# Kernel optimization log

Measured on AMD Instinct MI355X. Metric: run time of the kernel, lower is better.

The kernel has to match this reference:

```python
import jax, jax.numpy as jnp
import numpy as np

L_SIDE = 32
N_PIX = 12 * L_SIDE * L_SIDE      # 12288 sphere pixels
N_VALID = N_PIX // 2              # theta <= pi/2 hemisphere (first half by construction)
A_TH, B_TH, C_TH = 0.03, 1.0, 1.0  # ellipsoid semi-axes (thickness, 1, 1)


def _sphere_angles(n):
    # Deterministic Fibonacci-lattice sphere sampling standing in for SphereHealpix.
    i = np.arange(n, dtype=np.float64)
    z = 1.0 - 2.0 * (i + 0.5) / n          # cos(theta), descending -> theta<=pi/2 iff i < n/2
    theta = np.arccos(z)
    phi = (i * np.pi * (3.0 - np.sqrt(5.0))) % (2.0 * np.pi)
    return theta.astype(np.float32), phi.astype(np.float32)


def _ellipse_valid():
    # Faithful translation of ReconstructionModel.ellipse_valid for the valid hemisphere.
    theta_all, phi_all = _sphere_angles(N_PIX)
    tv = theta_all[:N_VALID].astype(np.float32)
    pv = phi_all[:N_VALID].astype(np.float32)
    a, b, c = np.float32(A_TH), np.float32(B_TH), np.float32(C_TH)
    # cartesian coords of valid pixels (computed BEFORE the angle shift)
    xv = np.cos(pv) * np.sin(tv)
    yv = np.sin(pv) * np.sin(tv)
    # meshgrid(phi, x) / meshgrid(theta, y) with ij indexing -> angles vary on rows, coords on cols
    phi = ((pv + np.pi / 2) % (2 * np.pi)).astype(np.float32)[:, None]   # [Nv,1]
    theta = ((tv + np.pi / 2) % np.pi).astype(np.float32)[:, None]       # [Nv,1]
    x = xv[None, :]
    y = yv[None, :]
    x_c = np.sin(2 * theta) / 2 * np.cos(phi)
    y_c = -np.sin(2 * theta) / 2 * np.sin(phi)
    z_c = (np.cos(2 * theta) + 1) / 2
    r = np.sqrt(2 * (np.cos(2 * theta) + 1)) / 2 + np.float32(1e-5)
    a2, b2, c2 = a * a, b * b, c * c
    ct, st = np.cos(theta), np.sin(theta)
    cp, sp = np.cos(phi), np.sin(phi)
    ct2, ct4 = ct ** 2, ct ** 4
    cp2 = cp ** 2
    x2, y2 = x ** 2, y ** 2
    s2p = np.sin(2.0 * phi)
    with np.errstate(invalid='ignore'):
        S = (-b2 * ct2 + b2 * ct4 - b2 * y2 - c2 * x2
             + a2 * b2 * ct4 + b2 * c2 * ct2 - b2 * c2 * ct4
             - b2 * x2 * cp2 + b2 * y2 * cp2 + c2 * x2 * cp2 - c2 * y2 * cp2
             - a2 * x2 * ct2 + c2 * x2 * ct2
             + b2 * x * y * s2p - c2 * x * y * s2p
             + a2 * x2 * cp2 * ct2 - a2 * y2 * cp2 * ct2
             - c2 * x2 * cp2 * ct2 + c2 * y2 * cp2 * ct2
             + 2.0 * b2 * x * cp * ct * st - 2.0 * b2 * y * ct * sp * st
             + 2.0 * c2 * x * y * cp * ct2 * sp - 2.0 * a2 * x * y * cp * ct2 * sp)
        num = (a * c * np.sqrt(S)
               - a2 * b * ct2 + 2.0 * a2 * b * ct4
               + 2.0 * b * c2 * ct2 - 2.0 * b * c2 * ct4
               + a2 * b * x * cp * ct * st - b * c2 * x * cp * ct * st
               - a2 * b * y * ct * sp * st + b * c2 * y * ct * sp * st)
        den = b * (a2 * ct2 - c2 * ct2 + c2)
        z = num / den
        f = ((x - x_c) ** 2 + (y - y_c) ** 2 + (z - z_c) ** 2) / r ** 2
    f = np.where(np.isnan(f), np.float32(0.0), f)   # f[f != f] = 0
    return f.astype(np.float32)


def setup_inputs() -> dict:
    key = jax.random.key(0)
    x = jax.random.uniform(key, (8, 16, N_PIX), dtype=jnp.float32)
    all_responses = jnp.asarray(_ellipse_valid())   # [N_VALID, N_VALID]
    return {"x": x, "all_responses": all_responses}


def reference(x, all_responses):
    nv = all_responses.shape[0]
    # masked gather: theta <= pi/2 is exactly the first nv pixels by construction
    x_valid = x[:, :, :nv]                                   # [B,C,Nv]
    mixture = jnp.einsum('bcn,nm->bcm', x_valid, all_responses)
    mixture = jnp.clip(mixture, 0.0, 1.0)                    # mix='clip'
    # masked scatter back into zero buffer
    out = jnp.zeros_like(x).at[:, :, :nv].set(mixture)
    return out
```

## Files before the change

kernel.cpp:

```cpp
#include <hip/hip_runtime.h>
#include <hip/hip_bf16.h>


#define NPIX 12288
#define NV   6144
#define MR   128
#define BNW  32
#define KST  128
#define NSTR (NV / BNW)
#define PARTF ((size_t)MR * NV)

typedef __attribute__((ext_vector_type(8))) short bf16x8;
typedef __attribute__((ext_vector_type(4))) float f32x4;
typedef __attribute__((ext_vector_type(4))) unsigned u32x4;

__device__ __forceinline__ unsigned pk2(float lo, float hi) {
    __hip_bfloat162 h = __float22bfloat162_rn(make_float2(lo, hi));
    union { __hip_bfloat162 h; unsigned u; } v; v.h = h; return v.u;
}

__device__ __forceinline__ void gld16(const void* g, void* l) {
    __builtin_amdgcn_global_load_lds(
        (const __attribute__((address_space(1))) void*)g,
        (__attribute__((address_space(3))) void*)l, 16, 0, 0);
}

__global__ __launch_bounds__(256) void prep_kernel(const float* __restrict__ x,
                                                   unsigned short* __restrict__ abf) {
    int q = blockIdx.x * 256 + threadIdx.x;
    int m = q / (NV / 8);
    int r = q % (NV / 8);
    int k = r * 8;
    const float* src = x + (size_t)m * NPIX + k;
    f32x4 a = *(const f32x4*)(src);
    f32x4 b = *(const f32x4*)(src + 4);
    u32x4 o;
    o[0] = pk2(a[0], a[1]); o[1] = pk2(a[2], a[3]);
    o[2] = pk2(b[0], b[1]); o[3] = pk2(b[2], b[3]);
    *(u32x4*)(abf + (size_t)m * NV + k) = o;
}

__global__ __launch_bounds__(256) void trans_kernel(const float* __restrict__ R,
                                                    unsigned short* __restrict__ RT) {
    __shared__ float T[64][65];
    const int tid = threadIdx.x;
    const int kt = blockIdx.x % (NV / 64);
    const int nt = blockIdx.x / (NV / 64);
    const int k0 = kt * 64, n0 = nt * 64;
    const int colg = (tid & 15) * 4;
    const int rowb = tid >> 4;
    #pragma unroll
    for (int it = 0; it < 4; ++it) {
        const int row = it * 16 + rowb;
        f32x4 v = *(const f32x4*)(R + (size_t)(k0 + row) * NV + n0 + colg);
        #pragma unroll
        for (int j = 0; j < 4; ++j) T[colg + j][row] = v[j];
    }
    __syncthreads();
    const int n = tid >> 2, seg = tid & 3;
    float f[16];
    #pragma unroll
    for (int u = 0; u < 16; ++u) f[u] = T[n][seg * 16 + u];
    u32x4 o0, o1;
    o0[0] = pk2(f[0], f[1]);  o0[1] = pk2(f[2], f[3]);
    o0[2] = pk2(f[4], f[5]);  o0[3] = pk2(f[6], f[7]);
    o1[0] = pk2(f[8], f[9]);  o1[1] = pk2(f[10], f[11]);
    o1[2] = pk2(f[12], f[13]); o1[3] = pk2(f[14], f[15]);
    unsigned short* dst = RT + (size_t)(n0 + n) * NV + k0 + seg * 16;
    *(u32x4*)(dst) = o0;
    *(u32x4*)(dst + 8) = o1;
}

__global__ __launch_bounds__(256) void gemm2_kernel(
        const unsigned short* __restrict__ A,
        const unsigned short* __restrict__ RT,
        float* __restrict__ out, float* __restrict__ wpart) {
    __shared__ unsigned char Bs[2][8192];

    const int tid = threadIdx.x;
    const int w = tid >> 6, l = tid & 63;
    const int ln = l & 15, lg = l >> 4;
    const int chunk = blockIdx.x & 7;
    const int nb = blockIdx.x >> 3;
    const int n0 = nb * BNW;
    const int kbase = chunk * 768;
    const int nsi = 768 / KST;

    const int f0 = tid * 16, f1 = 4096 + tid * 16;
    const int n_0 = f0 >> 8, n_1 = f1 >> 8;
    const int ko0 = (f0 & 255) ^ ((n_0 & 7) << 4);
    const int ko1 = (f1 & 255) ^ ((n_1 & 7) << 4);
    const char* g0 = (const char*)(RT + (size_t)(n0 + n_0) * NV + kbase) + ko0;
    const char* g1 = (const char*)(RT + (size_t)(n0 + n_1) * NV + kbase) + ko1;

    size_t arow0 = (size_t)(w * 32 + ln) * NV + kbase + lg * 8;
    size_t arow1 = arow0 + (size_t)16 * NV;

    f32x4 acc[2][2];
    #pragma unroll
    for (int a = 0; a < 2; ++a)
        #pragma unroll
        for (int b = 0; b < 2; ++b) {
            acc[a][b][0] = 0.f; acc[a][b][1] = 0.f;
            acc[a][b][2] = 0.f; acc[a][b][3] = 0.f;
        }

    gld16(g0, &Bs[0][f0]);
    gld16(g1, &Bs[0][f1]);
    __syncthreads();

    const int swn = (ln & 7) << 4;
    #pragma unroll 1
    for (int t = 0; t < nsi; ++t) {
        if (t + 1 < nsi) {
            const int nb2 = (t + 1) & 1;
            gld16(g0 + (t + 1) * 256, &Bs[nb2][f0]);
            gld16(g1 + (t + 1) * 256, &Bs[nb2][f1]);
        }
        const unsigned char* buf = Bs[t & 1];
        bf16x8 afr[2][4];
        #pragma unroll
        for (int ks = 0; ks < 4; ++ks) {
            afr[0][ks] = *(const bf16x8*)(A + arow0 + ks * 32);
            afr[1][ks] = *(const bf16x8*)(A + arow1 + ks * 32);
        }
        #pragma unroll
        for (int nt = 0; nt < 2; ++nt) {
            const int rowb = (nt * 16 + ln) * 256;
            #pragma unroll
            for (int ks = 0; ks < 4; ++ks) {
                bf16x8 bfr = *(const bf16x8*)(buf + rowb + (((lg * 16) + ks * 64) ^ swn));
                acc[0][nt] = __builtin_amdgcn_mfma_f32_16x16x32_bf16(afr[0][ks], bfr, acc[0][nt], 0, 0, 0);
                acc[1][nt] = __builtin_amdgcn_mfma_f32_16x16x32_bf16(afr[1][ks], bfr, acc[1][nt], 0, 0, 0);
            }
        }
        arow0 += KST; arow1 += KST;
        __syncthreads();
    }

    float* dst;
    size_t rstride;
    if (chunk < 2) { dst = out + (size_t)chunk * NV; rstride = NPIX; }
    else           { dst = wpart + (size_t)(chunk - 2) * PARTF; rstride = NV; }
    #pragma unroll
    for (int mt = 0; mt < 2; ++mt) {
        const int mbase = w * 32 + mt * 16 + lg * 4;
        #pragma unroll
        for (int nt = 0; nt < 2; ++nt) {
            const size_t cb = (size_t)(n0 + nt * 16 + ln);
            #pragma unroll
            for (int j = 0; j < 4; ++j)
                dst[(size_t)(mbase + j) * rstride + cb] = acc[mt][nt][j];
        }
    }
}

__device__ __forceinline__ bf16x8 cvt8(f32x4 a, f32x4 b) {
    union { unsigned u[4]; bf16x8 v; } r;
    r.u[0] = pk2(a[0], a[1]); r.u[1] = pk2(a[2], a[3]);
    r.u[2] = pk2(b[0], b[1]); r.u[3] = pk2(b[2], b[3]);
    return r.v;
}

__device__ __forceinline__ void sload(const float*& bptr, float2 (&r)[8]) {
    #pragma unroll
    for (int gi = 0; gi < 4; ++gi) {
        const float* p = bptr + (size_t)(gi * 32) * NV;
        r[2 * gi]     = *(const float2*)(p);
        r[2 * gi + 1] = *(const float2*)(p + NV);
    }
    bptr += (size_t)KST * NV;
}

__device__ __forceinline__ void wstage(unsigned char* buf, const float2 (&r)[8],
                                       int kq, int nq, int sw0, int sw1) {
    #pragma unroll
    for (int gi = 0; gi < 4; ++gi) {
        unsigned lo = pk2(r[2 * gi].x, r[2 * gi + 1].x);
        unsigned hi = pk2(r[2 * gi].y, r[2 * gi + 1].y);
        const int kbyte = (kq + gi * 32) * 2;
        *(unsigned*)(buf + nq * 256       + (kbyte ^ sw0)) = lo;
        *(unsigned*)(buf + (nq + 1) * 256 + (kbyte ^ sw1)) = hi;
    }
}

__device__ __forceinline__ void compute_fb(const unsigned char* buf,
        const float* __restrict__ X, size_t arow0, size_t arow1,
        int ln, int lg, f32x4 (&acc)[2][2]) {
    bf16x8 afr[2][4];
    #pragma unroll
    for (int ks = 0; ks < 4; ++ks) {
        f32x4 p0 = *(const f32x4*)(X + arow0 + ks * 32);
        f32x4 p1 = *(const f32x4*)(X + arow0 + ks * 32 + 4);
        afr[0][ks] = cvt8(p0, p1);
        f32x4 q0 = *(const f32x4*)(X + arow1 + ks * 32);
        f32x4 q1 = *(const f32x4*)(X + arow1 + ks * 32 + 4);
        afr[1][ks] = cvt8(q0, q1);
    }
    const int swn = (ln & 7) << 4;
    #pragma unroll
    for (int nt = 0; nt < 2; ++nt) {
        const int rowb = (nt * 16 + ln) * 256;
        #pragma unroll
        for (int ks = 0; ks < 4; ++ks) {
            bf16x8 bfr = *(const bf16x8*)(buf + rowb + (((lg * 16) + ks * 64) ^ swn));
            acc[0][nt] = __builtin_amdgcn_mfma_f32_16x16x32_bf16(afr[0][ks], bfr, acc[0][nt], 0, 0, 0);
            acc[1][nt] = __builtin_amdgcn_mfma_f32_16x16x32_bf16(afr[1][ks], bfr, acc[1][nt], 0, 0, 0);
        }
    }
}

__global__ __launch_bounds__(256) void gemm_fb_kernel(const float* __restrict__ X,
        const float* __restrict__ R, float* __restrict__ out) {
    __shared__ unsigned char Bs0[32 * 256];
    __shared__ unsigned char Bs1[32 * 256];
    const int tid = threadIdx.x;
    const int w = tid >> 6, l = tid & 63;
    const int ln = l & 15, lg = l >> 4;
    const int chunk = blockIdx.x / NSTR;
    const int nb = blockIdx.x % NSTR;
    const int n0 = nb * BNW;
    const int kbase = chunk * (NV / 2);
    const int nsi = (NV / 2) / KST;
    const int kq = (tid >> 4) * 2;
    const int nq = (tid & 15) * 2;
    const float* bptr = R + (size_t)(kbase + kq) * NV + (n0 + nq);
    const int sw0 = (nq & 7) << 4;
    const int sw1 = ((nq + 1) & 7) << 4;
    size_t arow0 = (size_t)(w * 32 + ln) * NPIX + kbase + lg * 8;
    size_t arow1 = arow0 + (size_t)16 * NPIX;
    f32x4 acc[2][2];
    #pragma unroll
    for (int a = 0; a < 2; ++a)
        #pragma unroll
        for (int b = 0; b < 2; ++b) {
            acc[a][b][0] = 0.f; acc[a][b][1] = 0.f;
            acc[a][b][2] = 0.f; acc[a][b][3] = 0.f;
        }
    float2 ring0[8], ring1[8];
    sload(bptr, ring0);
    sload(bptr, ring1);
    wstage(Bs0, ring0, kq, nq, sw0, sw1);
    __syncthreads();
    #pragma unroll 1
    for (int it = 0; it < nsi / 2; ++it) {
        const int s = it * 2;
        if (s + 2 < nsi) sload(bptr, ring0);
        compute_fb(Bs0, X, arow0, arow1, ln, lg, acc);
        arow0 += KST; arow1 += KST;
        wstage(Bs1, ring1, kq, nq, sw0, sw1);
        __syncthreads();
        if (s + 3 < nsi) sload(bptr, ring1);
        compute_fb(Bs1, X, arow0, arow1, ln, lg, acc);
        arow0 += KST; arow1 += KST;
        if (s + 2 < nsi) wstage(Bs0, ring0, kq, nq, sw0, sw1);
        __syncthreads();
    }
    float* dst = out + (size_t)chunk * NV;
    #pragma unroll
    for (int mt = 0; mt < 2; ++mt) {
        const int mbase = w * 32 + mt * 16 + lg * 4;
        #pragma unroll
        for (int nt = 0; nt < 2; ++nt) {
            const size_t cb = (size_t)(n0 + nt * 16 + ln);
            #pragma unroll
            for (int j = 0; j < 4; ++j)
                dst[(size_t)(mbase + j) * NPIX + cb] = acc[mt][nt][j];
        }
    }
}

__global__ __launch_bounds__(256) void reduce_kernel(float* __restrict__ out,
        const float* __restrict__ wpart, int nextra) {
    int q = blockIdx.x * 256 + threadIdx.x;
    int m = q / (NV / 4);
    int r = q % (NV / 4);
    size_t base = (size_t)m * NPIX + r * 4;
    f32x4 a = *(f32x4*)(out + base);
    f32x4 b = *(f32x4*)(out + base + NV);
    #pragma unroll
    for (int i = 0; i < 4; ++i) a[i] += b[i];
    #pragma unroll 1
    for (int p = 0; p < nextra; ++p) {
        f32x4 c = *(const f32x4*)(wpart + (size_t)p * PARTF + (size_t)m * NV + r * 4);
        #pragma unroll
        for (int i = 0; i < 4; ++i) a[i] += c[i];
    }
    f32x4 cz, z;
    #pragma unroll
    for (int i = 0; i < 4; ++i) {
        cz[i] = fminf(fmaxf(a[i], 0.f), 1.f);
        z[i] = 0.f;
    }
    *(f32x4*)(out + base) = cz;
    *(f32x4*)(out + base + NV) = z;
}

extern "C" void kernel_launch(void* const* d_in, const int* in_sizes, int n_in,
                              void* d_out, int out_size, void* d_ws, size_t ws_size,
                              hipStream_t stream) {
    const float* x = (const float*)d_in[0];
    const float* R = (const float*)d_in[1];
    float* out = (float*)d_out;

    const size_t abytes  = (size_t)MR * NV * 2;
    const size_t rtbytes = (size_t)NV * NV * 2;
    const size_t pbytes  = 6 * PARTF * 4;

    if (ws_size >= abytes + rtbytes + pbytes) {
        unsigned short* abf = (unsigned short*)d_ws;
        unsigned short* rt  = (unsigned short*)((char*)d_ws + abytes);
        float* wpart = (float*)((char*)d_ws + abytes + rtbytes);
        prep_kernel<<<(MR * NV / 8) / 256, 256, 0, stream>>>(x, abf);
        trans_kernel<<<(NV / 64) * (NV / 64), 256, 0, stream>>>(R, rt);
        gemm2_kernel<<<NSTR * 8, 256, 0, stream>>>(abf, rt, out, wpart);
        reduce_kernel<<<(MR * NV / 4) / 256, 256, 0, stream>>>(out, wpart, 6);
    } else {
        gemm_fb_kernel<<<NSTR * 2, 256, 0, stream>>>(x, R, out);
        reduce_kernel<<<(MR * NV / 4) / 256, 256, 0, stream>>>(out, nullptr, 0);
    }
}
```

Baseline: 278.6 us.

## Widen GEMM N tile, pad leading dims, rewrite transpose without LDS

The transpose kernel now reads eight rows of R per thread with vector loads and writes packed bf16 columns directly, with no shared-memory staging. The bf16 buffers and partials use a padded leading dimension of 6208 so that row strides avoid cache and channel aliasing. The GEMM tile grows from 32 to 64 N columns per block, so each A fragment is reused across more MFMAs, and the block count halves. All eight K-chunks now write partials to the workspace and a single reduce sums them, clamps and zero-fills, at the cost of more partial-buffer traffic and a larger workspace requirement.

```diff
diff --git a/kernel.cpp b/kernel.cpp
--- a/kernel.cpp
+++ b/kernel.cpp
@@ -5,10 +5,11 @@
 #define NPIX 12288
 #define NV   6144
 #define MR   128
-#define BNW  32
 #define KST  128
-#define NSTR (NV / BNW)
-#define PARTF ((size_t)MR * NV)
+#define LDK  6208
+#define LDA  6208
+#define LDP  6208
+#define PARTF ((size_t)MR * LDP)
 
 typedef __attribute__((ext_vector_type(8))) short bf16x8;
 typedef __attribute__((ext_vector_type(4))) float f32x4;
@@ -37,76 +38,71 @@
     u32x4 o;
     o[0] = pk2(a[0], a[1]); o[1] = pk2(a[2], a[3]);
     o[2] = pk2(b[0], b[1]); o[3] = pk2(b[2], b[3]);
-    *(u32x4*)(abf + (size_t)m * NV + k) = o;
+    *(u32x4*)(abf + (size_t)m * LDA + k) = o;
 }
 
 __global__ __launch_bounds__(256) void trans_kernel(const float* __restrict__ R,
                                                     unsigned short* __restrict__ RT) {
-    __shared__ float T[64][65];
     const int tid = threadIdx.x;
-    const int kt = blockIdx.x % (NV / 64);
-    const int nt = blockIdx.x / (NV / 64);
-    const int k0 = kt * 64, n0 = nt * 64;
-    const int colg = (tid & 15) * 4;
-    const int rowb = tid >> 4;
-    #pragma unroll
-    for (int it = 0; it < 4; ++it) {
-        const int row = it * 16 + rowb;
-        f32x4 v = *(const f32x4*)(R + (size_t)(k0 + row) * NV + n0 + colg);
-        #pragma unroll
-        for (int j = 0; j < 4; ++j) T[colg + j][row] = v[j];
-    }
-    __syncthreads();
-    const int n = tid >> 2, seg = tid & 3;
-    float f[16];
-    #pragma unroll
-    for (int u = 0; u < 16; ++u) f[u] = T[n][seg * 16 + u];
-    u32x4 o0, o1;
-    o0[0] = pk2(f[0], f[1]);  o0[1] = pk2(f[2], f[3]);
-    o0[2] = pk2(f[4], f[5]);  o0[3] = pk2(f[6], f[7]);
-    o1[0] = pk2(f[8], f[9]);  o1[1] = pk2(f[10], f[11]);
-    o1[2] = pk2(f[12], f[13]); o1[3] = pk2(f[14], f[15]);
-    unsigned short* dst = RT + (size_t)(n0 + n) * NV + k0 + seg * 16;
-    *(u32x4*)(dst) = o0;
-    *(u32x4*)(dst + 8) = o1;
+    const int w = tid >> 6, l = tid & 63;
+    const int band = blockIdx.x % 192;
+    const int nc   = blockIdx.x / 192;
+    const int k0 = band * 32 + w * 8;
+    const int n0 = nc * 256 + l * 4;
+    const float* src = R + (size_t)k0 * NV + n0;
+    f32x4 r[8];
+    #pragma unroll
+    for (int j = 0; j < 8; ++j) r[j] = *(const f32x4*)(src + (size_t)j * NV);
+    #pragma unroll
+    for (int c = 0; c < 4; ++c) {
+        u32x4 o;
+        o[0] = pk2(r[0][c], r[1][c]);
+        o[1] = pk2(r[2][c], r[3][c]);
+        o[2] = pk2(r[4][c], r[5][c]);
+        o[3] = pk2(r[6][c], r[7][c]);
+        *(u32x4*)(RT + (size_t)(n0 + c) * LDK + k0) = o;
+    }
 }
 
 __global__ __launch_bounds__(256) void gemm2_kernel(
         const unsigned short* __restrict__ A,
         const unsigned short* __restrict__ RT,
-        float* __restrict__ out, float* __restrict__ wpart) {
-    __shared__ unsigned char Bs[2][8192];
+        float* __restrict__ wpart) {
+    __shared__ unsigned char Bs[2][16384];
 
     const int tid = threadIdx.x;
     const int w = tid >> 6, l = tid & 63;
     const int ln = l & 15, lg = l >> 4;
     const int chunk = blockIdx.x & 7;
     const int nb = blockIdx.x >> 3;
-    const int n0 = nb * BNW;
+    const int n0 = nb * 64;
     const int kbase = chunk * 768;
     const int nsi = 768 / KST;
 
-    const int f0 = tid * 16, f1 = 4096 + tid * 16;
-    const int n_0 = f0 >> 8, n_1 = f1 >> 8;
-    const int ko0 = (f0 & 255) ^ ((n_0 & 7) << 4);
-    const int ko1 = (f1 & 255) ^ ((n_1 & 7) << 4);
-    const char* g0 = (const char*)(RT + (size_t)(n0 + n_0) * NV + kbase) + ko0;
-    const char* g1 = (const char*)(RT + (size_t)(n0 + n_1) * NV + kbase) + ko1;
-
-    size_t arow0 = (size_t)(w * 32 + ln) * NV + kbase + lg * 8;
-    size_t arow1 = arow0 + (size_t)16 * NV;
-
-    f32x4 acc[2][2];
+    int fo[4], nn[4];
+    const char* gg[4];
+    #pragma unroll
+    for (int i = 0; i < 4; ++i) {
+        fo[i] = tid * 16 + i * 4096;
+        nn[i] = fo[i] >> 8;
+        const int ko = (fo[i] & 255) ^ ((nn[i] & 7) << 4);
+        gg[i] = (const char*)(RT + (size_t)(n0 + nn[i]) * LDK + kbase) + ko;
+    }
+
+    size_t arow0 = (size_t)(w * 32 + ln) * LDA + kbase + lg * 8;
+    size_t arow1 = arow0 + (size_t)16 * LDA;
+
+    f32x4 acc[2][4];
     #pragma unroll
     for (int a = 0; a < 2; ++a)
         #pragma unroll
-        for (int b = 0; b < 2; ++b) {
+        for (int b = 0; b < 4; ++b) {
             acc[a][b][0] = 0.f; acc[a][b][1] = 0.f;
             acc[a][b][2] = 0.f; acc[a][b][3] = 0.f;
         }
 
-    gld16(g0, &Bs[0][f0]);
-    gld16(g1, &Bs[0][f1]);
+    #pragma unroll
+    for (int i = 0; i < 4; ++i) gld16(gg[i], &Bs[0][fo[i]]);
     __syncthreads();
 
     const int swn = (ln & 7) << 4;
@@ -114,8 +110,8 @@
     for (int t = 0; t < nsi; ++t) {
         if (t + 1 < nsi) {
             const int nb2 = (t + 1) & 1;
-            gld16(g0 + (t + 1) * 256, &Bs[nb2][f0]);
-            gld16(g1 + (t + 1) * 256, &Bs[nb2][f1]);
+            #pragma unroll
+            for (int i = 0; i < 4; ++i) gld16(gg[i] + (t + 1) * 256, &Bs[nb2][fo[i]]);
         }
         const unsigned char* buf = Bs[t & 1];
         bf16x8 afr[2][4];
@@ -125,7 +121,7 @@
             afr[1][ks] = *(const bf16x8*)(A + arow1 + ks * 32);
         }
         #pragma unroll
-        for (int nt = 0; nt < 2; ++nt) {
+        for (int nt = 0; nt < 4; ++nt) {
             const int rowb = (nt * 16 + ln) * 256;
             #pragma unroll
             for (int ks = 0; ks < 4; ++ks) {
@@ -138,41 +134,61 @@
         __syncthreads();
     }
 
-    float* dst;
-    size_t rstride;
-    if (chunk < 2) { dst = out + (size_t)chunk * NV; rstride = NPIX; }
-    else           { dst = wpart + (size_t)(chunk - 2) * PARTF; rstride = NV; }
+    float* dst = wpart + (size_t)chunk * PARTF;
     #pragma unroll
     for (int mt = 0; mt < 2; ++mt) {
         const int mbase = w * 32 + mt * 16 + lg * 4;
         #pragma unroll
-        for (int nt = 0; nt < 2; ++nt) {
+        for (int nt = 0; nt < 4; ++nt) {
             const size_t cb = (size_t)(n0 + nt * 16 + ln);
             #pragma unroll
             for (int j = 0; j < 4; ++j)
-                dst[(size_t)(mbase + j) * rstride + cb] = acc[mt][nt][j];
-        }
-    }
-}
-
+                dst[(size_t)(mbase + j) * LDP + cb] = acc[mt][nt][j];
+        }
+    }
+}
+
+__global__ __launch_bounds__(256) void reduce_kernel(float* __restrict__ out,
+        const float* __restrict__ wpart) {
+    int q = blockIdx.x * 256 + threadIdx.x;
+    int m = q / (NV / 4);
+    int r = q % (NV / 4);
+    f32x4 a;
+    a[0] = 0.f; a[1] = 0.f; a[2] = 0.f; a[3] = 0.f;
+    #pragma unroll 1
+    for (int p = 0; p < 8; ++p) {
+        f32x4 c = *(const f32x4*)(wpart + (size_t)p * PARTF + (size_t)m * LDP + r * 4);
+        #pragma unroll
+        for (int i = 0; i < 4; ++i) a[i] += c[i];
+    }
+    f32x4 cz, z;
+    #pragma unroll
+    for (int i = 0; i < 4; ++i) {
+        cz[i] = fminf(fmaxf(a[i], 0.f), 1.f);
+        z[i] = 0.f;
+    }
+    size_t base = (size_t)m * NPIX + r * 4;
+    *(f32x4*)(out + base) = cz;
+    *(f32x4*)(out + base + NV) = z;
+}
+
+typedef float2 fl2;
 __device__ __forceinline__ bf16x8 cvt8(f32x4 a, f32x4 b) {
     union { unsigned u[4]; bf16x8 v; } r;
     r.u[0] = pk2(a[0], a[1]); r.u[1] = pk2(a[2], a[3]);
     r.u[2] = pk2(b[0], b[1]); r.u[3] = pk2(b[2], b[3]);
     return r.v;
 }
-
-__device__ __forceinline__ void sload(const float*& bptr, float2 (&r)[8]) {
+__device__ __forceinline__ void sload(const float*& bptr, fl2 (&r)[8]) {
     #pragma unroll
     for (int gi = 0; gi < 4; ++gi) {
         const float* p = bptr + (size_t)(gi * 32) * NV;
-        r[2 * gi]     = *(const float2*)(p);
-        r[2 * gi + 1] = *(const float2*)(p + NV);
+        r[2 * gi]     = *(const fl2*)(p);
+        r[2 * gi + 1] = *(const fl2*)(p + NV);
     }
     bptr += (size_t)KST * NV;
 }
-
-__device__ __forceinline__ void wstage(unsigned char* buf, const float2 (&r)[8],
+__device__ __forceinline__ void wstage(unsigned char* buf, const fl2 (&r)[8],
                                        int kq, int nq, int sw0, int sw1) {
     #pragma unroll
     for (int gi = 0; gi < 4; ++gi) {
@@ -183,7 +199,6 @@
         *(unsigned*)(buf + (nq + 1) * 256 + (kbyte ^ sw1)) = hi;
     }
 }
-
 __device__ __forceinline__ void compute_fb(const unsigned char* buf,
         const float* __restrict__ X, size_t arow0, size_t arow1,
         int ln, int lg, f32x4 (&acc)[2][2]) {
@@ -209,7 +224,6 @@
         }
     }
 }
-
 __global__ __launch_bounds__(256) void gemm_fb_kernel(const float* __restrict__ X,
         const float* __restrict__ R, float* __restrict__ out) {
     __shared__ unsigned char Bs0[32 * 256];
@@ -217,9 +231,9 @@
     const int tid = threadIdx.x;
     const int w = tid >> 6, l = tid & 63;
     const int ln = l & 15, lg = l >> 4;
-    const int chunk = blockIdx.x / NSTR;
-    const int nb = blockIdx.x % NSTR;
-    const int n0 = nb * BNW;
+    const int chunk = blockIdx.x / 192;
+    const int nb = blockIdx.x % 192;
+    const int n0 = nb * 32;
     const int kbase = chunk * (NV / 2);
     const int nsi = (NV / 2) / KST;
     const int kq = (tid >> 4) * 2;
@@ -237,7 +251,7 @@
             acc[a][b][0] = 0.f; acc[a][b][1] = 0.f;
             acc[a][b][2] = 0.f; acc[a][b][3] = 0.f;
         }
-    float2 ring0[8], ring1[8];
+    fl2 ring0[8], ring1[8];
     sload(bptr, ring0);
     sload(bptr, ring1);
     wstage(Bs0, ring0, kq, nq, sw0, sw1);
@@ -269,27 +283,18 @@
         }
     }
 }
-
-__global__ __launch_bounds__(256) void reduce_kernel(float* __restrict__ out,
-        const float* __restrict__ wpart, int nextra) {
+__global__ __launch_bounds__(256) void reduce_fb_kernel(float* __restrict__ out) {
     int q = blockIdx.x * 256 + threadIdx.x;
     int m = q / (NV / 4);
     int r = q % (NV / 4);
     size_t base = (size_t)m * NPIX + r * 4;
     f32x4 a = *(f32x4*)(out + base);
     f32x4 b = *(f32x4*)(out + base + NV);
-    #pragma unroll
-    for (int i = 0; i < 4; ++i) a[i] += b[i];
-    #pragma unroll 1
-    for (int p = 0; p < nextra; ++p) {
-        f32x4 c = *(const f32x4*)(wpart + (size_t)p * PARTF + (size_t)m * NV + r * 4);
-        #pragma unroll
-        for (int i = 0; i < 4; ++i) a[i] += c[i];
-    }
     f32x4 cz, z;
     #pragma unroll
     for (int i = 0; i < 4; ++i) {
-        cz[i] = fminf(fmaxf(a[i], 0.f), 1.f);
+        float v = a[i] + b[i];
+        cz[i] = fminf(fmaxf(v, 0.f), 1.f);
         z[i] = 0.f;
     }
     *(f32x4*)(out + base) = cz;
@@ -303,20 +308,20 @@
     const float* R = (const float*)d_in[1];
     float* out = (float*)d_out;
 
-    const size_t abytes  = (size_t)MR * NV * 2;
-    const size_t rtbytes = (size_t)NV * NV * 2;
-    const size_t pbytes  = 6 * PARTF * 4;
-
-    if (ws_size >= abytes + rtbytes + pbytes) {
+    const size_t abytes  = (size_t)MR * LDA * 2;
+    const size_t rtbytes = (size_t)NV * LDK * 2;
+    const size_t wbytes  = 8 * PARTF * 4;
+
+    if (ws_size >= abytes + rtbytes + wbytes) {
         unsigned short* abf = (unsigned short*)d_ws;
         unsigned short* rt  = (unsigned short*)((char*)d_ws + abytes);
         float* wpart = (float*)((char*)d_ws + abytes + rtbytes);
         prep_kernel<<<(MR * NV / 8) / 256, 256, 0, stream>>>(x, abf);
-        trans_kernel<<<(NV / 64) * (NV / 64), 256, 0, stream>>>(R, rt);
-        gemm2_kernel<<<NSTR * 8, 256, 0, stream>>>(abf, rt, out, wpart);
-        reduce_kernel<<<(MR * NV / 4) / 256, 256, 0, stream>>>(out, wpart, 6);
+        trans_kernel<<<192 * 24, 256, 0, stream>>>(R, rt);
+        gemm2_kernel<<<96 * 8, 256, 0, stream>>>(abf, rt, wpart);
+        reduce_kernel<<<(MR * NV / 4) / 256, 256, 0, stream>>>(out, wpart);
     } else {
-        gemm_fb_kernel<<<NSTR * 2, 256, 0, stream>>>(x, R, out);
-        reduce_kernel<<<(MR * NV / 4) / 256, 256, 0, stream>>>(out, nullptr, 0);
-    }
-}
+        gemm_fb_kernel<<<192 * 2, 256, 0, stream>>>(x, R, out);
+        reduce_fb_kernel<<<(MR * NV / 4) / 256, 256, 0, stream>>>(out);
+    }
+}
```

Measured after the change: 292.9 us. +5.1%, slower.
